# Optimization experiments

Hardware: AMD Instinct MI355X
Metric: run time of the kernel (lower is better)

## Reference

```python
import jax, jax.numpy as jnp
import numpy as np

N = 100000      # nodes
E = 1600000     # edges
H = 128         # hidden_dim
L = 4           # num_layers (blocks AND inner GGC steps)
G = 512         # graphs in batch
IN = 128        # input_dim
OUT = 16        # output_dim
HS = H // 2     # mlp hidden


def setup_inputs() -> dict:
    key = jax.random.key(0)
    ks = jax.random.split(key, 24)
    s = 0.05
    inp = {
        "node_embed": jax.random.normal(ks[0], (N, IN), dtype=jnp.float32),
        "edge_index": jax.random.randint(ks[1], (2, E), 0, N, dtype=jnp.int32),
        "batch": jnp.sort(jax.random.randint(ks[2], (N,), 0, G, dtype=jnp.int32)),
        # nodeEmbed Linear
        "node_w": jax.random.normal(ks[3], (H, IN), dtype=jnp.float32) * s,
        "node_b": jnp.zeros((H,), dtype=jnp.float32),
        # per-block GatedGraphConv weights: [blocks, steps, H, H]
        "ggc_weight": jax.random.normal(ks[4], (L, L, H, H), dtype=jnp.float32) * s,
        # per-block GRUCell weights (torch layout: [3H, H], gates r,z,n)
        "gru_w_ih": jax.random.normal(ks[5], (L, 3 * H, H), dtype=jnp.float32) * s,
        "gru_w_hh": jax.random.normal(ks[6], (L, 3 * H, H), dtype=jnp.float32) * s,
        "gru_b_ih": jnp.zeros((L, 3 * H), dtype=jnp.float32),
        "gru_b_hh": jnp.zeros((L, 3 * H), dtype=jnp.float32),
        # cat_linear: H*L -> H
        "cat_w": jax.random.normal(ks[7], (H, H * L), dtype=jnp.float32) * s,
        "cat_b": jnp.zeros((H,), dtype=jnp.float32),
        # gate_nn: H -> 1
        "gate_w": jax.random.normal(ks[8], (1, H), dtype=jnp.float32) * s,
        "gate_b": jnp.zeros((1,), dtype=jnp.float32),
        # mlp
        "mlp_w1": jax.random.normal(ks[9], (HS, H), dtype=jnp.float32) * s,
        "mlp_b1": jnp.zeros((HS,), dtype=jnp.float32),
        "mlp_w2": jax.random.normal(ks[10], (HS, HS), dtype=jnp.float32) * s,
        "mlp_b2": jnp.zeros((HS,), dtype=jnp.float32),
        # heads
        "out_w": jax.random.normal(ks[11], (OUT, HS), dtype=jnp.float32) * s,
        "out_b": jnp.zeros((OUT,), dtype=jnp.float32),
        "line_w": jax.random.normal(ks[12], (OUT, H), dtype=jnp.float32) * s,
        "line_b": jnp.zeros((OUT,), dtype=jnp.float32),
    }
    return inp


def _gru_cell(m, h, w_ih, w_hh, b_ih, b_hh):
    gi = m @ w_ih.T + b_ih            # [N, 3H]
    gh = h @ w_hh.T + b_hh            # [N, 3H]
    i_r, i_z, i_n = jnp.split(gi, 3, axis=-1)
    h_r, h_z, h_n = jnp.split(gh, 3, axis=-1)
    r = jax.nn.sigmoid(i_r + h_r)
    z = jax.nn.sigmoid(i_z + h_z)
    n = jnp.tanh(i_n + r * h_n)
    return (1.0 - z) * n + z * h


def _gated_graph_conv(x, src, dst, W, w_ih, w_hh, b_ih, b_hh):
    n = x.shape[0]
    for i in range(W.shape[0]):       # fixed small step count
        m = x @ W[i]                  # [N, H]
        agg = jax.ops.segment_sum(m[src], dst, num_segments=n)  # scatter-add messages
        x = _gru_cell(agg, x, w_ih, w_hh, b_ih, b_hh)
    return x


def reference(node_embed, edge_index, batch, node_w, node_b, ggc_weight,
              gru_w_ih, gru_w_hh, gru_b_ih, gru_b_hh, cat_w, cat_b,
              gate_w, gate_b, mlp_w1, mlp_b1, mlp_w2, mlp_b2,
              out_w, out_b, line_w, line_b):
    src, dst = edge_index[0], edge_index[1]
    h0 = node_embed @ node_w.T + node_b                     # nodeEmbed
    # all residual blocks consume the SAME h0 (per original forward loop)
    outs = [
        _gated_graph_conv(h0, src, dst, ggc_weight[k], gru_w_ih[k],
                          gru_w_hh[k], gru_b_ih[k], gru_b_hh[k]) + h0
        for k in range(ggc_weight.shape[0])
    ]
    hidden = jnp.concatenate(outs, axis=-1) @ cat_w.T + cat_b  # [N, H]
    lineout = hidden @ line_w.T + line_b                       # [N, OUT]
    # attentional aggregation: scatter softmax over per-graph gates
    gate = (hidden @ gate_w.T + gate_b)[:, 0]                  # [N]
    gmax = jax.ops.segment_max(gate, batch, num_segments=G)
    ex = jnp.exp(gate - gmax[batch])
    denom = jax.ops.segment_sum(ex, batch, num_segments=G)
    alpha = ex / denom[batch]
    pooled = jax.ops.segment_sum(alpha[:, None] * hidden, batch, num_segments=G)  # [G, H]
    h = jax.nn.relu(pooled @ mlp_w1.T + mlp_b1)
    h = jax.nn.relu(h @ mlp_w2.T + mlp_b2)
    out = h @ out_w.T + out_b                                  # [G, OUT]
    return (out, lineout)
```

## Files before the change

### kernel.cpp

```cpp
#include <hip/hip_runtime.h>

#define N_NODES 100000
#define N_EDGES 1600000
#define HD 128
#define NH (N_NODES * HD)

typedef __attribute__((ext_vector_type(8))) short bf16x8;
typedef __attribute__((ext_vector_type(4))) float f32x4;

__device__ inline unsigned short f2bf(float f) {
  unsigned u = __float_as_uint(f);
  unsigned r = (u + 0x7FFFu + ((u >> 16) & 1u)) >> 16;
  return (unsigned short)r;
}
__device__ inline float bf2f(unsigned short b) {
  return __uint_as_float(((unsigned)b) << 16);
}
__device__ inline float sigm_f(float x) {
  return __builtin_amdgcn_rcpf(1.f + __expf(-x));
}
__device__ inline float tanh_f(float x) {
  return 1.f - 2.f * __builtin_amdgcn_rcpf(__expf(2.f * x) + 1.f);
}

__global__ __launch_bounds__(256) void gemm_h0_k(
    const float* __restrict__ A, const float* __restrict__ B,
    const float* __restrict__ bias, unsigned short* __restrict__ Cb, int M) {
  __shared__ float As[16][132];
  __shared__ float Bs[16][68];
  const int tid = threadIdx.x;
  const int row0 = blockIdx.x * 128;
  const int col0 = blockIdx.y * 64;
  const int tx = tid & 15, ty = tid >> 4;

  float acc[8][4];
#pragma unroll
  for (int i = 0; i < 8; i++)
#pragma unroll
    for (int j = 0; j < 4; j++) acc[i][j] = 0.f;

  const int lr = tid >> 2;
  const int kg = (tid & 3) * 4;

  for (int k0 = 0; k0 < 128; k0 += 16) {
#pragma unroll
    for (int h = 0; h < 2; ++h) {
      int r = lr + h * 64;
      float4 v = make_float4(0.f, 0.f, 0.f, 0.f);
      if (row0 + r < M)
        v = *reinterpret_cast<const float4*>(A + (size_t)(row0 + r) * 128 + k0 + kg);
      As[kg + 0][r] = v.x;
      As[kg + 1][r] = v.y;
      As[kg + 2][r] = v.z;
      As[kg + 3][r] = v.w;
    }
    {
      int c = lr;
      float4 v = *reinterpret_cast<const float4*>(B + (size_t)(col0 + c) * 128 + k0 + kg);
      Bs[kg + 0][c] = v.x;
      Bs[kg + 1][c] = v.y;
      Bs[kg + 2][c] = v.z;
      Bs[kg + 3][c] = v.w;
    }
    __syncthreads();
#pragma unroll
    for (int kk = 0; kk < 16; ++kk) {
      float a[8], b[4];
#pragma unroll
      for (int i = 0; i < 8; i++) a[i] = As[kk][ty * 8 + i];
#pragma unroll
      for (int j = 0; j < 4; j++) b[j] = Bs[kk][tx * 4 + j];
#pragma unroll
      for (int i = 0; i < 8; i++)
#pragma unroll
        for (int j = 0; j < 4; j++) acc[i][j] += a[i] * b[j];
    }
    __syncthreads();
  }

#pragma unroll
  for (int i = 0; i < 8; i++) {
    int r = row0 + ty * 8 + i;
    if (r < M) {
#pragma unroll
      for (int j = 0; j < 4; j++) {
        int c = col0 + tx * 4 + j;
        Cb[(size_t)r * 128 + c] = f2bf(acc[i][j] + bias[c]);
      }
    }
  }
}

__global__ __launch_bounds__(256) void gemm_wct_k(
    const float* __restrict__ w_ih, const float* __restrict__ ggc_w,
    float* __restrict__ Cout) {
  const int z = blockIdx.z;
  const float* A = w_ih + (size_t)(z >> 2) * 384 * 128;
  const float* B = ggc_w + (size_t)z * 128 * 128;
  float* C = Cout + (size_t)z * 384 * 128;
  __shared__ float As[16][132];
  __shared__ float Bs[16][68];
  const int tid = threadIdx.x;
  const int row0 = blockIdx.x * 128;
  const int col0 = blockIdx.y * 64;
  const int tx = tid & 15, ty = tid >> 4;

  float acc[8][4];
#pragma unroll
  for (int i = 0; i < 8; i++)
#pragma unroll
    for (int j = 0; j < 4; j++) acc[i][j] = 0.f;

  const int lr = tid >> 2;
  const int kg = (tid & 3) * 4;

  for (int k0 = 0; k0 < 128; k0 += 16) {
#pragma unroll
    for (int h = 0; h < 2; ++h) {
      int r = lr + h * 64;
      float4 v = *reinterpret_cast<const float4*>(A + (size_t)(row0 + r) * 128 + k0 + kg);
      As[kg + 0][r] = v.x;
      As[kg + 1][r] = v.y;
      As[kg + 2][r] = v.z;
      As[kg + 3][r] = v.w;
    }
    {
      int c = lr;
      float4 v = *reinterpret_cast<const float4*>(B + (size_t)(col0 + c) * 128 + k0 + kg);
      Bs[kg + 0][c] = v.x;
      Bs[kg + 1][c] = v.y;
      Bs[kg + 2][c] = v.z;
      Bs[kg + 3][c] = v.w;
    }
    __syncthreads();
#pragma unroll
    for (int kk = 0; kk < 16; ++kk) {
      float a[8], b[4];
#pragma unroll
      for (int i = 0; i < 8; i++) a[i] = As[kk][ty * 8 + i];
#pragma unroll
      for (int j = 0; j < 4; j++) b[j] = Bs[kk][tx * 4 + j];
#pragma unroll
      for (int i = 0; i < 8; i++)
#pragma unroll
        for (int j = 0; j < 4; j++) acc[i][j] += a[i] * b[j];
    }
    __syncthreads();
  }

#pragma unroll
  for (int i = 0; i < 8; i++) {
    int r = row0 + ty * 8 + i;
#pragma unroll
    for (int j = 0; j < 4; j++) {
      int c = col0 + tx * 4 + j;
      C[(size_t)r * 128 + c] = acc[i][j];
    }
  }
}

__global__ __launch_bounds__(256) void f2b_k(const float* __restrict__ a,
                                             unsigned short* __restrict__ b, int n) {
  int i = blockIdx.x * 256 + threadIdx.x;
  if (i * 4 >= n) return;
  float4 v = reinterpret_cast<const float4*>(a)[i];
  ushort4 o;
  o.x = f2bf(v.x);
  o.y = f2bf(v.y);
  o.z = f2bf(v.z);
  o.w = f2bf(v.w);
  reinterpret_cast<ushort4*>(b)[i] = o;
}

template <bool LAST>
__global__ __launch_bounds__(512) void gru_mfma7_k(
    const unsigned short* __restrict__ agg_base, size_t agg_zs,
    const unsigned short* __restrict__ xb_base, size_t xb_zs,
    const unsigned short* __restrict__ h0b,
    const unsigned short* __restrict__ wct_base, size_t wct_zs,
    const unsigned short* __restrict__ whh_base, size_t whh_zs,
    const float* __restrict__ bih_base, const float* __restrict__ bhh_base,
    unsigned short* __restrict__ Xout, int nRowTiles) {
  const int z = blockIdx.y;
  const unsigned short* agg = agg_base + (size_t)z * agg_zs;
  const unsigned short* xb = xb_base + (size_t)z * xb_zs;
  unsigned short* out = Xout + (size_t)z * NH;
  const unsigned short* wctb = wct_base + (size_t)z * wct_zs;
  const unsigned short* whhb = whh_base + (size_t)z * whh_zs;
  const float* b_ih = bih_base + z * 384;
  const float* b_hh = bhh_base + z * 384;

  const int lane = threadIdx.x & 63;
  const int wave = threadIdx.x >> 6;
  const int lrow = lane & 15;
  const int kblk = lane >> 4;
  const int c = wave * 16 + lrow;

  bf16x8 wf[6][4];
#pragma unroll
  for (int s = 0; s < 3; s++)
#pragma unroll
    for (int kk = 0; kk < 4; kk++) {
      size_t off = (size_t)(s * 128 + c) * 128 + kk * 32 + kblk * 8;
      wf[s][kk] = *reinterpret_cast<const bf16x8*>(wctb + off);
      wf[s + 3][kk] = *reinterpret_cast<const bf16x8*>(whhb + off);
    }
  const float bi0 = b_ih[c], bi1 = b_ih[128 + c], bi2 = b_ih[256 + c];
  const float bh0 = b_hh[c], bh1 = b_hh[128 + c], bh2 = b_hh[256 + c];

  for (int rt = blockIdx.x; rt < nRowTiles; rt += gridDim.x) {
    const int row0 = rt * 16;
    const size_t abase = (size_t)(row0 + lrow) * 128 + kblk * 8;

    f32x4 acc[6];
#pragma unroll
    for (int s = 0; s < 6; s++) acc[s] = (f32x4)(0.f);
#pragma unroll
    for (int kk = 0; kk < 4; kk++) {
      bf16x8 a_ag = *reinterpret_cast<const bf16x8*>(agg + abase + kk * 32);
      bf16x8 a_x = *reinterpret_cast<const bf16x8*>(xb + abase + kk * 32);
      acc[0] = __builtin_amdgcn_mfma_f32_16x16x32_bf16(a_ag, wf[0][kk], acc[0], 0, 0, 0);
      acc[1] = __builtin_amdgcn_mfma_f32_16x16x32_bf16(a_ag, wf[1][kk], acc[1], 0, 0, 0);
      acc[2] = __builtin_amdgcn_mfma_f32_16x16x32_bf16(a_ag, wf[2][kk], acc[2], 0, 0, 0);
      acc[3] = __builtin_amdgcn_mfma_f32_16x16x32_bf16(a_x, wf[3][kk], acc[3], 0, 0, 0);
      acc[4] = __builtin_amdgcn_mfma_f32_16x16x32_bf16(a_x, wf[4][kk], acc[4], 0, 0, 0);
      acc[5] = __builtin_amdgcn_mfma_f32_16x16x32_bf16(a_x, wf[5][kk], acc[5], 0, 0, 0);
    }
    __syncthreads();
#pragma unroll
    for (int r = 0; r < 4; r++) {
      int orow = row0 + kblk * 4 + r;
      size_t idx = (size_t)orow * 128 + c;
      float ir = acc[0][r] + bi0;
      float iz = acc[1][r] + bi1;
      float in_ = acc[2][r] + bi2;
      float hr = acc[3][r] + bh0;
      float hz = acc[4][r] + bh1;
      float hn = acc[5][r] + bh2;
      float rg = sigm_f(ir + hr);
      float zg = sigm_f(iz + hz);
      float ng = tanh_f(in_ + rg * hn);
      float h = bf2f(xb[idx]);
      float nv = (1.f - zg) * ng + zg * h;
      if (LAST) nv += bf2f(h0b[idx]);
      out[idx] = f2bf(nv);
    }
  }
}

__global__ __launch_bounds__(256) void cat_full_k(
    const unsigned short* __restrict__ X,
    const unsigned short* __restrict__ wcatb,
    const float* __restrict__ cat_b, float* __restrict__ hidden, int M) {
  const int lane = threadIdx.x & 63;
  const int wave = threadIdx.x >> 6;
  const int row0 = blockIdx.x * 64 + wave * 16;
  const int c0 = blockIdx.y * 32;
  const int lrow = lane & 15;
  const int kb = lane >> 4;
  int arow = row0 + lrow;
  if (arow >= M) arow = M - 1;

  f32x4 acc[2];
  acc[0] = (f32x4)(0.f);
  acc[1] = (f32x4)(0.f);
#pragma unroll
  for (int kk = 0; kk < 16; kk++) {
    const unsigned short* ob = X + (size_t)(kk >> 2) * NH;
    bf16x8 a = *reinterpret_cast<const bf16x8*>(
        ob + (size_t)arow * 128 + (kk & 3) * 32 + kb * 8);
#pragma unroll
    for (int t = 0; t < 2; t++) {
      bf16x8 b = *reinterpret_cast<const bf16x8*>(
          wcatb + (size_t)(c0 + t * 16 + lrow) * 512 + (kk >> 2) * 128 +
          (kk & 3) * 32 + kb * 8);
      acc[t] = __builtin_amdgcn_mfma_f32_16x16x32_bf16(a, b, acc[t], 0, 0, 0);
    }
  }
#pragma unroll
  for (int r = 0; r < 4; r++) {
    int orow = row0 + kb * 4 + r;
    if (orow >= M) continue;
#pragma unroll
    for (int t = 0; t < 2; t++) {
      int c = c0 + t * 16 + lrow;
      hidden[(size_t)orow * 128 + c] = acc[t][r] + cat_b[c];
    }
  }
}

__global__ __launch_bounds__(256) void deg_hist_k(const int* __restrict__ dst,
                                                  int* __restrict__ deg) {
  int e = blockIdx.x * 256 + threadIdx.x;
  if (e >= N_EDGES) return;
  atomicAdd(&deg[dst[e]], 1);
}

__global__ __launch_bounds__(256) void scan1_k(const int* __restrict__ deg,
                                               int* __restrict__ offsets,
                                               int* __restrict__ bsum) {
  __shared__ int buf[256];
  int tid = threadIdx.x;
  int idx = blockIdx.x * 256 + tid;
  int v = (idx < N_NODES) ? deg[idx] : 0;
  buf[tid] = v;
  __syncthreads();
  for (int off = 1; off < 256; off <<= 1) {
    int t = (tid >= off) ? buf[tid - off] : 0;
    __syncthreads();
    buf[tid] += t;
    __syncthreads();
  }
  if (idx < N_NODES) offsets[idx] = buf[tid] - v;
  if (tid == 255) bsum[blockIdx.x] = buf[255];
}

__global__ __launch_bounds__(512) void scan2_k(int* __restrict__ bsum, int nb) {
  __shared__ int buf[512];
  int tid = threadIdx.x;
  int v = (tid < nb) ? bsum[tid] : 0;
  buf[tid] = v;
  __syncthreads();
  for (int off = 1; off < 512; off <<= 1) {
    int t = (tid >= off) ? buf[tid - off] : 0;
    __syncthreads();
    buf[tid] += t;
    __syncthreads();
  }
  if (tid < nb) bsum[tid] = buf[tid] - v;
}

__global__ __launch_bounds__(256) void scan3_k(int* __restrict__ offsets,
                                               const int* __restrict__ bsum) {
  int idx = blockIdx.x * 256 + threadIdx.x;
  if (idx < N_NODES) offsets[idx] += bsum[idx >> 8];
  if (idx == 0) offsets[N_NODES] = N_EDGES;
}

__global__ __launch_bounds__(256) void copy_int_k(const int* __restrict__ a,
                                                  int* __restrict__ b, int n) {
  int i = blockIdx.x * 256 + threadIdx.x;
  if (i < n) b[i] = a[i];
}

__global__ __launch_bounds__(256) void fill_k(const int* __restrict__ src,
                                              const int* __restrict__ dst,
                                              int* __restrict__ cursor,
                                              int* __restrict__ srcs_sorted) {
  int e = blockIdx.x * 256 + threadIdx.x;
  if (e >= N_EDGES) return;
  int pos = atomicAdd(&cursor[dst[e]], 1);
  srcs_sorted[pos] = src[e];
}

__global__ __launch_bounds__(256) void gather5_k(
    const unsigned short* __restrict__ xb_base, size_t xstride,
    const int* __restrict__ offsets, const int* __restrict__ srcs,
    unsigned short* __restrict__ aggb, int nz) {
  int wid = (blockIdx.x * 256 + threadIdx.x) >> 6;
  int lane = threadIdx.x & 63;
  if (wid >= nz * N_NODES) return;
  int z = 0, node = wid;
  if (node >= 2 * N_NODES) { z = 2; node -= 2 * N_NODES; }
  if (node >= N_NODES) { z += 1; node -= N_NODES; }
  const unsigned short* xb = xb_base + (size_t)z * xstride;
  int beg = offsets[node], end = offsets[node + 1];
  int half = lane >> 5;
  int cg = (lane & 31) * 4;
  float a0 = 0.f, a1 = 0.f, a2 = 0.f, a3 = 0.f;
  int e = beg + half;
  for (; e + 6 < end; e += 8) {
    int s0 = srcs[e], s1 = srcs[e + 2], s2 = srcs[e + 4], s3 = srcs[e + 6];
    uint2 v0 = *reinterpret_cast<const uint2*>(xb + (size_t)s0 * 128 + cg);
    uint2 v1 = *reinterpret_cast<const uint2*>(xb + (size_t)s1 * 128 + cg);
    uint2 v2 = *reinterpret_cast<const uint2*>(xb + (size_t)s2 * 128 + cg);
    uint2 v3 = *reinterpret_cast<const uint2*>(xb + (size_t)s3 * 128 + cg);
    a0 += bf2f((unsigned short)(v0.x & 0xFFFFu)) + bf2f((unsigned short)(v1.x & 0xFFFFu)) +
          bf2f((unsigned short)(v2.x & 0xFFFFu)) + bf2f((unsigned short)(v3.x & 0xFFFFu));
    a1 += bf2f((unsigned short)(v0.x >> 16)) + bf2f((unsigned short)(v1.x >> 16)) +
          bf2f((unsigned short)(v2.x >> 16)) + bf2f((unsigned short)(v3.x >> 16));
    a2 += bf2f((unsigned short)(v0.y & 0xFFFFu)) + bf2f((unsigned short)(v1.y & 0xFFFFu)) +
          bf2f((unsigned short)(v2.y & 0xFFFFu)) + bf2f((unsigned short)(v3.y & 0xFFFFu));
    a3 += bf2f((unsigned short)(v0.y >> 16)) + bf2f((unsigned short)(v1.y >> 16)) +
          bf2f((unsigned short)(v2.y >> 16)) + bf2f((unsigned short)(v3.y >> 16));
  }
  for (; e < end; e += 2) {
    int s0 = srcs[e];
    uint2 v0 = *reinterpret_cast<const uint2*>(xb + (size_t)s0 * 128 + cg);
    a0 += bf2f((unsigned short)(v0.x & 0xFFFFu));
    a1 += bf2f((unsigned short)(v0.x >> 16));
    a2 += bf2f((unsigned short)(v0.y & 0xFFFFu));
    a3 += bf2f((unsigned short)(v0.y >> 16));
  }
  a0 += __shfl_down(a0, 32);
  a1 += __shfl_down(a1, 32);
  a2 += __shfl_down(a2, 32);
  a3 += __shfl_down(a3, 32);
  if (half == 0) {
    uint2 o;
    o.x = (unsigned)f2bf(a0) | ((unsigned)f2bf(a1) << 16);
    o.y = (unsigned)f2bf(a2) | ((unsigned)f2bf(a3) << 16);
    *reinterpret_cast<uint2*>(aggb + (size_t)z * NH + (size_t)node * 128 + cg) = o;
  }
}

__global__ __launch_bounds__(256) void lineout_k(
    const float* __restrict__ hidden, const float* __restrict__ W,
    const float* __restrict__ b, float* __restrict__ out) {
  __shared__ float Ws[16 * 128];
  for (int i = threadIdx.x; i < 2048; i += 256) Ws[i] = W[i];
  __syncthreads();
  int r = threadIdx.x >> 4, c = threadIdx.x & 15;
  int n = blockIdx.x * 16 + r;
  if (n >= N_NODES) return;
  const float* h = hidden + (size_t)n * 128;
  const float* w = Ws + c * 128;
  float acc = 0.f;
#pragma unroll 8
  for (int k = 0; k < 128; k++) acc += h[k] * w[k];
  out[(size_t)n * 16 + c] = acc + b[c];
}

__global__ __launch_bounds__(256) void gate_k(
    const float* __restrict__ hidden, const float* __restrict__ gw,
    const float* __restrict__ gb, float* __restrict__ gate) {
  int wid = (blockIdx.x * 256 + threadIdx.x) >> 6;
  int lane = threadIdx.x & 63;
  if (wid >= N_NODES) return;
  const float* h = hidden + (size_t)wid * 128;
  float s = h[lane] * gw[lane] + h[64 + lane] * gw[64 + lane];
#pragma unroll
  for (int off = 32; off; off >>= 1) s += __shfl_down(s, off);
  if (lane == 0) gate[wid] = s + gb[0];
}

__global__ void graph_start_k(const int* __restrict__ batch, int* __restrict__ gs) {
  int g = threadIdx.x;
  if (g > 512) return;
  if (g == 512) {
    gs[512] = N_NODES;
    return;
  }
  int lo = 0, hi = N_NODES;
  while (lo < hi) {
    int mid = (lo + hi) >> 1;
    if (batch[mid] < g) lo = mid + 1;
    else hi = mid;
  }
  gs[g] = lo;
}

__global__ __launch_bounds__(256) void pool_fused_k(
    const float* __restrict__ hidden, const float* __restrict__ gate,
    const int* __restrict__ gs, float* __restrict__ ex,
    float* __restrict__ pooled) {
  const int g = blockIdx.x;
  const int beg = gs[g], end = gs[g + 1];
  const int tid = threadIdx.x, lane = tid & 63, wv = tid >> 6;
  __shared__ float red[4];
  __shared__ float sval;
  __shared__ float colbuf[256];

  if (end <= beg) {
    if (tid < 128) pooled[(size_t)g * 128 + tid] = 0.f;
    return;
  }
  float m = -3.4e38f;
  for (int n = beg + tid; n < end; n += 256) m = fmaxf(m, gate[n]);
#pragma unroll
  for (int off = 32; off; off >>= 1) m = fmaxf(m, __shfl_down(m, off));
  if (lane == 0) red[wv] = m;
  __syncthreads();
  if (tid == 0) sval = fmaxf(fmaxf(red[0], red[1]), fmaxf(red[2], red[3]));
  __syncthreads();
  const float mx = sval;
  float s = 0.f;
  for (int n = beg + tid; n < end; n += 256) {
    float e = __expf(gate[n] - mx);
    ex[n] = e;
    s += e;
  }
#pragma unroll
  for (int off = 32; off; off >>= 1) s += __shfl_down(s, off);
  if (lane == 0) red[wv] = s;
  __syncthreads();
  if (tid == 0) sval = red[0] + red[1] + red[2] + red[3];
  __syncthreads();
  const float denom = sval;
  const int col = tid & 127, half = tid >> 7;
  float acc = 0.f;
  for (int n = beg + half; n < end; n += 2)
    acc += ex[n] * hidden[(size_t)n * 128 + col];
  colbuf[tid] = acc;
  __syncthreads();
  if (tid < 128)
    pooled[(size_t)g * 128 + tid] = (colbuf[tid] + colbuf[tid + 128]) / denom;
}

__global__ void mlp1_k(const float* __restrict__ pooled, const float* __restrict__ w,
                       const float* __restrict__ b, float* __restrict__ h1) {
  int g = blockIdx.x, j = threadIdx.x;
  const float* p = pooled + (size_t)g * 128;
  const float* wr = w + (size_t)j * 128;
  float acc = 0.f;
#pragma unroll 8
  for (int k = 0; k < 128; k++) acc += p[k] * wr[k];
  acc += b[j];
  h1[g * 64 + j] = acc > 0.f ? acc : 0.f;
}

__global__ void mlp2_k(const float* __restrict__ h1, const float* __restrict__ w,
                       const float* __restrict__ b, float* __restrict__ h2) {
  int g = blockIdx.x, j = threadIdx.x;
  const float* p = h1 + (size_t)g * 64;
  const float* wr = w + (size_t)j * 64;
  float acc = 0.f;
#pragma unroll 8
  for (int k = 0; k < 64; k++) acc += p[k] * wr[k];
  acc += b[j];
  h2[g * 64 + j] = acc > 0.f ? acc : 0.f;
}

__global__ void outhead_k(const float* __restrict__ h2, const float* __restrict__ w,
                          const float* __restrict__ b, float* __restrict__ out) {
  int g = blockIdx.x, j = threadIdx.x;
  if (j >= 16) return;
  const float* p = h2 + (size_t)g * 64;
  const float* wr = w + (size_t)j * 64;
  float acc = 0.f;
#pragma unroll 8
  for (int k = 0; k < 64; k++) acc += p[k] * wr[k];
  out[g * 16 + j] = acc + b[j];
}

extern "C" void kernel_launch(void* const* d_in, const int* in_sizes, int n_in,
                              void* d_out, int out_size, void* d_ws, size_t ws_size,
                              hipStream_t stream) {
  const float* node_embed = (const float*)d_in[0];
  const int* eidx = (const int*)d_in[1];
  const int* batch = (const int*)d_in[2];
  const float* node_w = (const float*)d_in[3];
  const float* node_b = (const float*)d_in[4];
  const float* ggc_w = (const float*)d_in[5];
  const float* w_ih = (const float*)d_in[6];
  const float* w_hh = (const float*)d_in[7];
  const float* b_ih = (const float*)d_in[8];
  const float* b_hh = (const float*)d_in[9];
  const float* cat_w = (const float*)d_in[10];
  const float* cat_b = (const float*)d_in[11];
  const float* gate_w = (const float*)d_in[12];
  const float* gate_b = (const float*)d_in[13];
  const float* mlp_w1 = (const float*)d_in[14];
  const float* mlp_b1 = (const float*)d_in[15];
  const float* mlp_w2 = (const float*)d_in[16];
  const float* mlp_b2 = (const float*)d_in[17];
  const float* out_w = (const float*)d_in[18];
  const float* out_b = (const float*)d_in[19];
  const float* line_w = (const float*)d_in[20];
  const float* line_b = (const float*)d_in[21];

  const int* src = eidx;
  const int* dst = eidx + N_EDGES;

  unsigned short* h0b = (unsigned short*)d_ws;
  unsigned short* X = h0b + (size_t)NH;
  unsigned short* aggb = X + (size_t)4 * NH;
  unsigned short* wctb = aggb + (size_t)4 * NH;
  unsigned short* whhb = wctb + 16 * 384 * 128;
  unsigned short* wcatb = whhb + 4 * 384 * 128;
  int* offsets = (int*)(wcatb + 128 * 512);
  int* cursor = offsets + N_NODES + 1;
  int* srcs_sorted = cursor + N_NODES;
  int* bsum = srcs_sorted + N_EDGES;
  int* gs = bsum + 512;
  float* WcTf = (float*)aggb;
  float* hidden = (float*)aggb;

  float* out_graph = (float*)d_out;
  float* out_line = (float*)d_out + 512 * 16;

  dim3 blk(256);
  const int gM128 = (N_NODES + 127) / 128;
  const int gM64 = (N_NODES + 63) / 64;
  const int gE = (N_EDGES + 255) / 256;
  const int nScanBlk = (N_NODES + 255) / 256;
  const int nRowTiles = N_NODES / 16;
  const size_t S = (size_t)384 * 128;

  hipMemsetAsync(cursor, 0, N_NODES * sizeof(int), stream);
  deg_hist_k<<<gE, blk, 0, stream>>>(dst, cursor);
  scan1_k<<<nScanBlk, blk, 0, stream>>>(cursor, offsets, bsum);
  scan2_k<<<1, 512, 0, stream>>>(bsum, nScanBlk);
  scan3_k<<<nScanBlk, blk, 0, stream>>>(offsets, bsum);
  copy_int_k<<<(N_NODES + 255) / 256, blk, 0, stream>>>(offsets, cursor, N_NODES);
  fill_k<<<gE, blk, 0, stream>>>(src, dst, cursor, srcs_sorted);
  graph_start_k<<<1, 576, 0, stream>>>(batch, gs);

  gemm_wct_k<<<dim3(3, 2, 16), blk, 0, stream>>>(w_ih, ggc_w, WcTf);
  f2b_k<<<(16 * 384 * 128 / 4 + 255) / 256, blk, 0, stream>>>(WcTf, wctb, 16 * 384 * 128);
  f2b_k<<<(4 * 384 * 128 / 4 + 255) / 256, blk, 0, stream>>>(w_hh, whhb, 4 * 384 * 128);
  f2b_k<<<(128 * 512 / 4 + 255) / 256, blk, 0, stream>>>(cat_w, wcatb, 128 * 512);

  gemm_h0_k<<<dim3(gM128, 2), blk, 0, stream>>>(node_embed, node_w, node_b, h0b, N_NODES);

  const dim3 gruGrid(128, 4);
  for (int i = 0; i < 4; i++) {
    const unsigned short* xin = (i == 0) ? h0b : X;
    const size_t xzs = (i == 0) ? 0 : (size_t)NH;
    const int nz = (i == 0) ? 1 : 4;
    const size_t agg_zs = (i == 0) ? 0 : (size_t)NH;
    gather5_k<<<(nz * N_NODES * 64 + 255) / 256, blk, 0, stream>>>(
        xin, xzs, offsets, srcs_sorted, aggb, nz);
    const unsigned short* wct_i = wctb + (size_t)i * S;
    if (i < 3)
      gru_mfma7_k<false><<<gruGrid, 512, 0, stream>>>(
          aggb, agg_zs, xin, xzs, h0b, wct_i, 4 * S, whhb, S, b_ih, b_hh, X,
          nRowTiles);
    else
      gru_mfma7_k<true><<<gruGrid, 512, 0, stream>>>(
          aggb, agg_zs, xin, xzs, h0b, wct_i, 4 * S, whhb, S, b_ih, b_hh, X,
          nRowTiles);
  }

  cat_full_k<<<dim3(gM64, 4), blk, 0, stream>>>(X, wcatb, cat_b, hidden, N_NODES);

  lineout_k<<<(N_NODES + 15) / 16, blk, 0, stream>>>(hidden, line_w, line_b, out_line);

  float* gate = (float*)X;
  float* ex = (float*)X + N_NODES;
  float* pooled = hidden + (size_t)NH;
  float* h1 = pooled + 512 * 128;
  float* h2 = h1 + 512 * 64;

  gate_k<<<(N_NODES * 64 + 255) / 256, blk, 0, stream>>>(hidden, gate_w, gate_b, gate);
  pool_fused_k<<<512, blk, 0, stream>>>(hidden, gate, gs, ex, pooled);
  mlp1_k<<<512, 64, 0, stream>>>(pooled, mlp_w1, mlp_b1, h1);
  mlp2_k<<<512, 64, 0, stream>>>(h1, mlp_w2, mlp_b2, h2);
  outhead_k<<<512, 64, 0, stream>>>(h2, out_w, out_b, out_graph);
}
```

Before: 2.296 ms.

## Fuse neighbor gather into GRU MFMA kernel with ping-pong node-state buffers

For steps 2-4, each GRU block now gathers and sums neighbor features for its 16-row tile straight into swizzled, double-buffered LDS, then runs the MFMA GRU on them. This drops the separate gather kernel and the round trip of the aggregated tensor through global memory. Node states now alternate between two buffers instead of being updated in place, which removes the old per-tile barrier, and the grid grows from 128 to 1024 blocks per block index. In exchange, the GRU kernel does irregular gather work with only one wave per row and fewer edges in flight, so the matrix units may sit idle while it waits on memory latency.

```diff
diff --git a/kernel.cpp b/kernel.cpp
--- a/kernel.cpp
+++ b/kernel.cpp
@@ -172,19 +172,21 @@
   reinterpret_cast<ushort4*>(b)[i] = o;
 }
 
-template <bool LAST>
-__global__ __launch_bounds__(512) void gru_mfma7_k(
-    const unsigned short* __restrict__ agg_base, size_t agg_zs,
-    const unsigned short* __restrict__ xb_base, size_t xb_zs,
+template <bool GAGG, bool LAST>
+__global__ __launch_bounds__(512) void gru_fused8_k(
+    const unsigned short* __restrict__ agg_g, size_t agg_zs,
+    const unsigned short* __restrict__ Xin_base, size_t xin_zs,
     const unsigned short* __restrict__ h0b,
+    const int* __restrict__ offsets, const int* __restrict__ srcs,
     const unsigned short* __restrict__ wct_base, size_t wct_zs,
     const unsigned short* __restrict__ whh_base, size_t whh_zs,
     const float* __restrict__ bih_base, const float* __restrict__ bhh_base,
     unsigned short* __restrict__ Xout, int nRowTiles) {
+  __shared__ unsigned short aggs[2][16 * 128];
   const int z = blockIdx.y;
-  const unsigned short* agg = agg_base + (size_t)z * agg_zs;
-  const unsigned short* xb = xb_base + (size_t)z * xb_zs;
-  unsigned short* out = Xout + (size_t)z * NH;
+  const unsigned short* agg = agg_g + (size_t)z * agg_zs;
+  const unsigned short* xin = Xin_base + (size_t)z * xin_zs;
+  unsigned short* xout = Xout + (size_t)z * NH;
   const unsigned short* wctb = wct_base + (size_t)z * wct_zs;
   const unsigned short* whhb = whh_base + (size_t)z * whh_zs;
   const float* b_ih = bih_base + z * 384;
@@ -208,25 +210,67 @@
   const float bi0 = b_ih[c], bi1 = b_ih[128 + c], bi2 = b_ih[256 + c];
   const float bh0 = b_hh[c], bh1 = b_hh[128 + c], bh2 = b_hh[256 + c];
 
-  for (int rt = blockIdx.x; rt < nRowTiles; rt += gridDim.x) {
+  int buf = 0;
+  for (int rt = blockIdx.x; rt < nRowTiles; rt += gridDim.x, buf ^= 1) {
     const int row0 = rt * 16;
+
+    if (!GAGG) {
+#pragma unroll
+      for (int h = 0; h < 2; h++) {
+        const int lr = 2 * wave + h;
+        const int row = row0 + lr;
+        const int beg = offsets[row], end = offsets[row + 1];
+        float ax = 0.f, ay = 0.f;
+        int e = beg;
+        for (; e + 3 < end; e += 4) {
+          int s0 = srcs[e], s1 = srcs[e + 1], s2 = srcs[e + 2], s3 = srcs[e + 3];
+          unsigned v0 = *reinterpret_cast<const unsigned*>(xin + (size_t)s0 * 128 + lane * 2);
+          unsigned v1 = *reinterpret_cast<const unsigned*>(xin + (size_t)s1 * 128 + lane * 2);
+          unsigned v2 = *reinterpret_cast<const unsigned*>(xin + (size_t)s2 * 128 + lane * 2);
+          unsigned v3 = *reinterpret_cast<const unsigned*>(xin + (size_t)s3 * 128 + lane * 2);
+          ax += bf2f((unsigned short)(v0 & 0xFFFFu)) + bf2f((unsigned short)(v1 & 0xFFFFu)) +
+                bf2f((unsigned short)(v2 & 0xFFFFu)) + bf2f((unsigned short)(v3 & 0xFFFFu));
+          ay += bf2f((unsigned short)(v0 >> 16)) + bf2f((unsigned short)(v1 >> 16)) +
+                bf2f((unsigned short)(v2 >> 16)) + bf2f((unsigned short)(v3 >> 16));
+        }
+        for (; e < end; e++) {
+          int s0 = srcs[e];
+          unsigned v0 = *reinterpret_cast<const unsigned*>(xin + (size_t)s0 * 128 + lane * 2);
+          ax += bf2f((unsigned short)(v0 & 0xFFFFu));
+          ay += bf2f((unsigned short)(v0 >> 16));
+        }
+        unsigned o = (unsigned)f2bf(ax) | ((unsigned)f2bf(ay) << 16);
+        unsigned off = (unsigned)(lr * 256 + lane * 4) ^ (unsigned)((lr & 7) << 4);
+        *reinterpret_cast<unsigned*>(reinterpret_cast<char*>(aggs[buf]) + off) = o;
+      }
+      __syncthreads();
+    }
+
     const size_t abase = (size_t)(row0 + lrow) * 128 + kblk * 8;
+    bf16x8 a_ag[4], a_x[4];
+#pragma unroll
+    for (int kk = 0; kk < 4; kk++) {
+      if (GAGG) {
+        a_ag[kk] = *reinterpret_cast<const bf16x8*>(agg + abase + kk * 32);
+      } else {
+        unsigned off = (unsigned)(lrow * 256 + kk * 64 + kblk * 16) ^ (unsigned)((lrow & 7) << 4);
+        a_ag[kk] = *reinterpret_cast<const bf16x8*>(reinterpret_cast<char*>(aggs[buf]) + off);
+      }
+      a_x[kk] = *reinterpret_cast<const bf16x8*>(xin + abase + kk * 32);
+    }
 
     f32x4 acc[6];
 #pragma unroll
     for (int s = 0; s < 6; s++) acc[s] = (f32x4)(0.f);
 #pragma unroll
     for (int kk = 0; kk < 4; kk++) {
-      bf16x8 a_ag = *reinterpret_cast<const bf16x8*>(agg + abase + kk * 32);
-      bf16x8 a_x = *reinterpret_cast<const bf16x8*>(xb + abase + kk * 32);
-      acc[0] = __builtin_amdgcn_mfma_f32_16x16x32_bf16(a_ag, wf[0][kk], acc[0], 0, 0, 0);
-      acc[1] = __builtin_amdgcn_mfma_f32_16x16x32_bf16(a_ag, wf[1][kk], acc[1], 0, 0, 0);
-      acc[2] = __builtin_amdgcn_mfma_f32_16x16x32_bf16(a_ag, wf[2][kk], acc[2], 0, 0, 0);
-      acc[3] = __builtin_amdgcn_mfma_f32_16x16x32_bf16(a_x, wf[3][kk], acc[3], 0, 0, 0);
-      acc[4] = __builtin_amdgcn_mfma_f32_16x16x32_bf16(a_x, wf[4][kk], acc[4], 0, 0, 0);
-      acc[5] = __builtin_amdgcn_mfma_f32_16x16x32_bf16(a_x, wf[5][kk], acc[5], 0, 0, 0);
-    }
-    __syncthreads();
+      acc[0] = __builtin_amdgcn_mfma_f32_16x16x32_bf16(a_ag[kk], wf[0][kk], acc[0], 0, 0, 0);
+      acc[1] = __builtin_amdgcn_mfma_f32_16x16x32_bf16(a_ag[kk], wf[1][kk], acc[1], 0, 0, 0);
+      acc[2] = __builtin_amdgcn_mfma_f32_16x16x32_bf16(a_ag[kk], wf[2][kk], acc[2], 0, 0, 0);
+      acc[3] = __builtin_amdgcn_mfma_f32_16x16x32_bf16(a_x[kk], wf[3][kk], acc[3], 0, 0, 0);
+      acc[4] = __builtin_amdgcn_mfma_f32_16x16x32_bf16(a_x[kk], wf[4][kk], acc[4], 0, 0, 0);
+      acc[5] = __builtin_amdgcn_mfma_f32_16x16x32_bf16(a_x[kk], wf[5][kk], acc[5], 0, 0, 0);
+    }
 #pragma unroll
     for (int r = 0; r < 4; r++) {
       int orow = row0 + kblk * 4 + r;
@@ -240,17 +284,16 @@
       float rg = sigm_f(ir + hr);
       float zg = sigm_f(iz + hz);
       float ng = tanh_f(in_ + rg * hn);
-      float h = bf2f(xb[idx]);
+      float h = bf2f(xin[idx]);
       float nv = (1.f - zg) * ng + zg * h;
       if (LAST) nv += bf2f(h0b[idx]);
-      out[idx] = f2bf(nv);
+      xout[idx] = f2bf(nv);
     }
   }
 }
 
 __global__ __launch_bounds__(256) void cat_full_k(
-    const unsigned short* __restrict__ X,
-    const unsigned short* __restrict__ wcatb,
+    const unsigned short* __restrict__ X, const unsigned short* __restrict__ wcatb,
     const float* __restrict__ cat_b, float* __restrict__ hidden, int M) {
   const int lane = threadIdx.x & 63;
   const int wave = threadIdx.x >> 6;
@@ -354,16 +397,11 @@
 }
 
 __global__ __launch_bounds__(256) void gather5_k(
-    const unsigned short* __restrict__ xb_base, size_t xstride,
-    const int* __restrict__ offsets, const int* __restrict__ srcs,
-    unsigned short* __restrict__ aggb, int nz) {
-  int wid = (blockIdx.x * 256 + threadIdx.x) >> 6;
+    const unsigned short* __restrict__ xb, const int* __restrict__ offsets,
+    const int* __restrict__ srcs, unsigned short* __restrict__ aggb) {
+  int node = (blockIdx.x * 256 + threadIdx.x) >> 6;
   int lane = threadIdx.x & 63;
-  if (wid >= nz * N_NODES) return;
-  int z = 0, node = wid;
-  if (node >= 2 * N_NODES) { z = 2; node -= 2 * N_NODES; }
-  if (node >= N_NODES) { z += 1; node -= N_NODES; }
-  const unsigned short* xb = xb_base + (size_t)z * xstride;
+  if (node >= N_NODES) return;
   int beg = offsets[node], end = offsets[node + 1];
   int half = lane >> 5;
   int cg = (lane & 31) * 4;
@@ -400,7 +438,7 @@
     uint2 o;
     o.x = (unsigned)f2bf(a0) | ((unsigned)f2bf(a1) << 16);
     o.y = (unsigned)f2bf(a2) | ((unsigned)f2bf(a3) << 16);
-    *reinterpret_cast<uint2*>(aggb + (size_t)z * NH + (size_t)node * 128 + cg) = o;
+    *reinterpret_cast<uint2*>(aggb + (size_t)node * 128 + cg) = o;
   }
 }
 
@@ -563,9 +601,9 @@
   const int* dst = eidx + N_EDGES;
 
   unsigned short* h0b = (unsigned short*)d_ws;
-  unsigned short* X = h0b + (size_t)NH;
-  unsigned short* aggb = X + (size_t)4 * NH;
-  unsigned short* wctb = aggb + (size_t)4 * NH;
+  unsigned short* X0 = h0b + (size_t)NH;
+  unsigned short* X1 = X0 + (size_t)4 * NH;
+  unsigned short* wctb = X1 + (size_t)4 * NH;
   unsigned short* whhb = wctb + 16 * 384 * 128;
   unsigned short* wcatb = whhb + 4 * 384 * 128;
   int* offsets = (int*)(wcatb + 128 * 512);
@@ -573,8 +611,9 @@
   int* srcs_sorted = cursor + N_NODES;
   int* bsum = srcs_sorted + N_EDGES;
   int* gs = bsum + 512;
-  float* WcTf = (float*)aggb;
-  float* hidden = (float*)aggb;
+  float* WcTf = (float*)X0;
+  unsigned short* aggTmp = X1;
+  float* hidden = (float*)X0;
 
   float* out_graph = (float*)d_out;
   float* out_line = (float*)d_out + 512 * 16;
@@ -603,32 +642,28 @@
 
   gemm_h0_k<<<dim3(gM128, 2), blk, 0, stream>>>(node_embed, node_w, node_b, h0b, N_NODES);
 
-  const dim3 gruGrid(128, 4);
-  for (int i = 0; i < 4; i++) {
-    const unsigned short* xin = (i == 0) ? h0b : X;
-    const size_t xzs = (i == 0) ? 0 : (size_t)NH;
-    const int nz = (i == 0) ? 1 : 4;
-    const size_t agg_zs = (i == 0) ? 0 : (size_t)NH;
-    gather5_k<<<(nz * N_NODES * 64 + 255) / 256, blk, 0, stream>>>(
-        xin, xzs, offsets, srcs_sorted, aggb, nz);
-    const unsigned short* wct_i = wctb + (size_t)i * S;
-    if (i < 3)
-      gru_mfma7_k<false><<<gruGrid, 512, 0, stream>>>(
-          aggb, agg_zs, xin, xzs, h0b, wct_i, 4 * S, whhb, S, b_ih, b_hh, X,
-          nRowTiles);
-    else
-      gru_mfma7_k<true><<<gruGrid, 512, 0, stream>>>(
-          aggb, agg_zs, xin, xzs, h0b, wct_i, 4 * S, whhb, S, b_ih, b_hh, X,
-          nRowTiles);
-  }
-
-  cat_full_k<<<dim3(gM64, 4), blk, 0, stream>>>(X, wcatb, cat_b, hidden, N_NODES);
+  const dim3 G8(1024, 4);
+  gather5_k<<<(N_NODES * 64 + 255) / 256, blk, 0, stream>>>(h0b, offsets, srcs_sorted, aggTmp);
+  gru_fused8_k<true, false><<<G8, 512, 0, stream>>>(
+      aggTmp, 0, h0b, 0, h0b, offsets, srcs_sorted, wctb, 4 * S, whhb, S,
+      b_ih, b_hh, X0, nRowTiles);
+  gru_fused8_k<false, false><<<G8, 512, 0, stream>>>(
+      nullptr, 0, X0, NH, h0b, offsets, srcs_sorted, wctb + S, 4 * S, whhb, S,
+      b_ih, b_hh, X1, nRowTiles);
+  gru_fused8_k<false, false><<<G8, 512, 0, stream>>>(
+      nullptr, 0, X1, NH, h0b, offsets, srcs_sorted, wctb + 2 * S, 4 * S, whhb, S,
+      b_ih, b_hh, X0, nRowTiles);
+  gru_fused8_k<false, true><<<G8, 512, 0, stream>>>(
+      nullptr, 0, X0, NH, h0b, offsets, srcs_sorted, wctb + 3 * S, 4 * S, whhb, S,
+      b_ih, b_hh, X1, nRowTiles);
+
+  cat_full_k<<<dim3(gM64, 4), blk, 0, stream>>>(X1, wcatb, cat_b, hidden, N_NODES);
 
   lineout_k<<<(N_NODES + 15) / 16, blk, 0, stream>>>(hidden, line_w, line_b, out_line);
 
-  float* gate = (float*)X;
-  float* ex = (float*)X + N_NODES;
-  float* pooled = hidden + (size_t)NH;
+  float* gate = (float*)X1;
+  float* ex = (float*)X1 + N_NODES;
+  float* pooled = ex + N_NODES;
   float* h1 = pooled + 512 * 128;
   float* h2 = h1 + 512 * 64;
 
```

Result: slower. 3.954 ms (+72.2%).
